# Kernel optimization log

Measured on AMD Instinct MI355X. Metric: run time of the kernel, lower is better.

## Reference

```python
import jax, jax.numpy as jnp
import numpy as np

N_NODES = 4096
N_GRAPHS = 128
D_IN = 128
HEADS = 4
KEY_SIZE = 32  # == num_channels
D_OUT = 32 * D_IN  # num_channels * irreps.dim


def setup_inputs() -> dict:
    key = jax.random.key(0)
    ks = jax.random.split(key, 5)
    nodes = jax.random.normal(ks[0], (N_NODES, D_IN), dtype=jnp.float32)
    # 128 graphs of 32 nodes each, packed: sum(n_node) == N_NODES
    n_node = jnp.full((N_GRAPHS,), N_NODES // N_GRAPHS, dtype=jnp.int32)
    s_in = 1.0 / np.sqrt(D_IN)
    s_h = 1.0 / np.sqrt(HEADS * KEY_SIZE)
    Wq = jax.random.normal(ks[1], (D_IN, HEADS, KEY_SIZE), dtype=jnp.float32) * s_in
    Wk = jax.random.normal(ks[2], (D_IN, HEADS, KEY_SIZE), dtype=jnp.float32) * s_in
    Wv = jax.random.normal(ks[3], (D_IN, HEADS, KEY_SIZE), dtype=jnp.float32) * s_in
    Wo = jax.random.normal(ks[4], (HEADS * KEY_SIZE, D_OUT), dtype=jnp.float32) * s_h
    bq = jnp.zeros((HEADS, KEY_SIZE), dtype=jnp.float32)
    bk = jnp.zeros((HEADS, KEY_SIZE), dtype=jnp.float32)
    bv = jnp.zeros((HEADS, KEY_SIZE), dtype=jnp.float32)
    bo = jnp.zeros((D_OUT,), dtype=jnp.float32)
    return {"nodes": nodes, "n_node": n_node, "Wq": Wq, "bq": bq,
            "Wk": Wk, "bk": bk, "Wv": Wv, "bv": bv, "Wo": Wo, "bo": bo}


def reference(nodes, n_node, Wq, bq, Wk, bk, Wv, bv, Wo, bo):
    N = nodes.shape[0]
    G = n_node.shape[0]
    # segment id per packed node (get_segment_ids)
    seg = jnp.repeat(jnp.arange(G), n_node, total_repeat_length=N)
    # per-head projections: [N, H, K]
    q = jnp.einsum('nd,dhk->nhk', nodes, Wq) + bq
    k = jnp.einsum('nd,dhk->nhk', nodes, Wk) + bk
    v = jnp.einsum('nd,dhk->nhk', nodes, Wv) + bv
    # dense logits masked to block-diagonal per-graph blocks: [H, N, N]
    logits = jnp.einsum('nhk,mhk->hnm', q, k) / jnp.sqrt(jnp.float32(KEY_SIZE))
    mask = seg[:, None] == seg[None, :]  # [N, N]
    logits = jnp.where(mask[None, :, :], logits, jnp.float32(-1e30))
    attn = jax.nn.softmax(logits, axis=-1)
    out = jnp.einsum('hnm,mhk->nhk', attn, v).reshape(N, HEADS * KEY_SIZE)
    return out @ Wo + bo  # [N, num_channels * d_in]
```

## Files before the change

### kernel.cpp

```cpp
#include <hip/hip_runtime.h>
#include <hip/hip_bf16.h>


typedef __attribute__((ext_vector_type(4))) float f32x4;
typedef __attribute__((ext_vector_type(8))) short s16x8;
typedef __attribute__((ext_vector_type(4))) short s16x4;
typedef __attribute__((ext_vector_type(8))) __bf16 bf16x8;

static __device__ __forceinline__ short f2bf(float f) {
  union { float f; unsigned u; } v; v.f = f;
  unsigned r = v.u + 0x7fffu + ((v.u >> 16) & 1u);
  return (short)(r >> 16);
}

static __device__ __forceinline__ f32x4 mfma16(s16x8 a, s16x8 b, f32x4 c) {
  return __builtin_amdgcn_mfma_f32_16x16x32_bf16(
      __builtin_bit_cast(bf16x8, a), __builtin_bit_cast(bf16x8, b), c, 0, 0, 0);
}

__global__ __launch_bounds__(256) void k0_prep(
    const float* __restrict__ Wq, const float* __restrict__ Wk,
    const float* __restrict__ Wv, const float* __restrict__ Wo,
    unsigned short* __restrict__ WqkvT, unsigned short* __restrict__ WoT)
{
  __shared__ alignas(16) short sT[64][136];
  const int b = blockIdx.x;
  const float* in; unsigned short* out; int C; int n0;
  if (b < 64)      { in = Wo; out = WoT;           C = 4096; n0 = b << 6; }
  else if (b < 66) { in = Wq; out = WqkvT;         C = 128;  n0 = (b - 64) << 6; }
  else if (b < 68) { in = Wk; out = WqkvT + 16384; C = 128;  n0 = (b - 66) << 6; }
  else             { in = Wv; out = WqkvT + 32768; C = 128;  n0 = (b - 68) << 6; }
  const int t  = threadIdx.x;
  const int rr = t >> 4;
  const int c4 = (t & 15) << 2;
  #pragma unroll
  for (int i = 0; i < 8; ++i) {
    int r = i * 16 + rr;
    float4 v = *(const float4*)(in + r * C + n0 + c4);
    sT[c4 + 0][r] = f2bf(v.x);
    sT[c4 + 1][r] = f2bf(v.y);
    sT[c4 + 2][r] = f2bf(v.z);
    sT[c4 + 3][r] = f2bf(v.w);
  }
  __syncthreads();
  const int c  = t >> 2;
  const int k0 = (t & 3) << 5;
  #pragma unroll
  for (int j = 0; j < 4; ++j)
    *(s16x8*)&out[(n0 + c) * 128 + k0 + j * 8] = *(const s16x8*)&sT[c][k0 + j * 8];
}

__global__ __launch_bounds__(64) void k1_qkv_attn(
    const float* __restrict__ nodes,
    const unsigned short* __restrict__ WqkvT,
    const float* __restrict__ bq, const float* __restrict__ bk,
    const float* __restrict__ bv,
    unsigned short* __restrict__ attout)
{
  const int g = blockIdx.x;
  const int h = blockIdx.y;
  const int lane = threadIdx.x;
  const int l15 = lane & 15;
  const int qd = lane >> 4;

  __shared__ alignas(16) short sN[32][136];
  __shared__ alignas(16) short sQ[32][40];
  __shared__ alignas(16) short sK[32][40];
  __shared__ alignas(16) short sVT[32][40];
  __shared__ alignas(16) short sP[32][40];

  const float* ng = nodes + g * 32 * 128;
  #pragma unroll
  for (int i = 0; i < 16; ++i) {
    int f4  = i * 64 + lane;
    int row = f4 >> 5;
    int c4  = (f4 & 31) << 2;
    float4 v = *(const float4*)(ng + row * 128 + c4);
    s16x4 p;
    p[0] = f2bf(v.x); p[1] = f2bf(v.y); p[2] = f2bf(v.z); p[3] = f2bf(v.w);
    *(s16x4*)&sN[row][c4] = p;
  }
  __syncthreads();

  s16x8 afrag[2][4];
  #pragma unroll
  for (int mt = 0; mt < 2; ++mt)
    #pragma unroll
    for (int kk = 0; kk < 4; ++kk)
      afrag[mt][kk] = *(const s16x8*)&sN[mt * 16 + l15][kk * 32 + qd * 8];

  const float* Bm[3] = {bq, bk, bv};

  #pragma unroll
  for (int m3 = 0; m3 < 3; ++m3) {
    const unsigned short* WT = WqkvT + m3 * 16384;
    s16x8 bfr[4][2];
    #pragma unroll
    for (int kk = 0; kk < 4; ++kk)
      #pragma unroll
      for (int nt = 0; nt < 2; ++nt)
        bfr[kk][nt] = *(const s16x8*)&WT[(h * 32 + nt * 16 + l15) * 128 + kk * 32 + qd * 8];
    f32x4 acc[2][2];
    f32x4 zero = {0.f, 0.f, 0.f, 0.f};
    acc[0][0] = zero; acc[0][1] = zero; acc[1][0] = zero; acc[1][1] = zero;
    #pragma unroll
    for (int kk = 0; kk < 4; ++kk)
      #pragma unroll
      for (int mt = 0; mt < 2; ++mt)
        #pragma unroll
        for (int nt = 0; nt < 2; ++nt)
          acc[mt][nt] = mfma16(afrag[mt][kk], bfr[kk][nt], acc[mt][nt]);
    float b0 = Bm[m3][h * 32 + l15];
    float b1 = Bm[m3][h * 32 + 16 + l15];
    #pragma unroll
    for (int mt = 0; mt < 2; ++mt)
      #pragma unroll
      for (int nt = 0; nt < 2; ++nt) {
        float bb = nt ? b1 : b0;
        #pragma unroll
        for (int r = 0; r < 4; ++r) {
          int m = mt * 16 + qd * 4 + r;
          int c = nt * 16 + l15;
          float val = acc[mt][nt][r] + bb;
          if (m3 == 0)      sQ[m][c]  = f2bf(val * 0.17677669529663687f);
          else if (m3 == 1) sK[m][c]  = f2bf(val);
          else              sVT[c][m] = f2bf(val);
        }
      }
  }
  __syncthreads();

  s16x8 qf[2], kf[2];
  #pragma unroll
  for (int mt = 0; mt < 2; ++mt) qf[mt] = *(const s16x8*)&sQ[mt * 16 + l15][qd * 8];
  #pragma unroll
  for (int nt = 0; nt < 2; ++nt) kf[nt] = *(const s16x8*)&sK[nt * 16 + l15][qd * 8];
  f32x4 sacc[2][2];
  {
    f32x4 zero = {0.f, 0.f, 0.f, 0.f};
    #pragma unroll
    for (int mt = 0; mt < 2; ++mt)
      #pragma unroll
      for (int nt = 0; nt < 2; ++nt)
        sacc[mt][nt] = mfma16(qf[mt], kf[nt], zero);
  }

  #pragma unroll
  for (int mt = 0; mt < 2; ++mt)
    #pragma unroll
    for (int r = 0; r < 4; ++r) {
      float a0 = sacc[mt][0][r], a1 = sacc[mt][1][r];
      float mx = fmaxf(a0, a1);
      mx = fmaxf(mx, __shfl_xor(mx, 1, 64));
      mx = fmaxf(mx, __shfl_xor(mx, 2, 64));
      mx = fmaxf(mx, __shfl_xor(mx, 4, 64));
      mx = fmaxf(mx, __shfl_xor(mx, 8, 64));
      float e0 = __expf(a0 - mx), e1 = __expf(a1 - mx);
      float s = e0 + e1;
      s += __shfl_xor(s, 1, 64);
      s += __shfl_xor(s, 2, 64);
      s += __shfl_xor(s, 4, 64);
      s += __shfl_xor(s, 8, 64);
      float inv = 1.0f / s;
      int m = mt * 16 + qd * 4 + r;
      sP[m][l15]      = f2bf(e0 * inv);
      sP[m][16 + l15] = f2bf(e1 * inv);
    }
  __syncthreads();

  s16x8 pf[2], vf[2];
  #pragma unroll
  for (int mt = 0; mt < 2; ++mt) pf[mt] = *(const s16x8*)&sP[mt * 16 + l15][qd * 8];
  #pragma unroll
  for (int nt = 0; nt < 2; ++nt) vf[nt] = *(const s16x8*)&sVT[nt * 16 + l15][qd * 8];
  f32x4 oacc[2][2];
  {
    f32x4 zero = {0.f, 0.f, 0.f, 0.f};
    #pragma unroll
    for (int mt = 0; mt < 2; ++mt)
      #pragma unroll
      for (int nt = 0; nt < 2; ++nt)
        oacc[mt][nt] = mfma16(pf[mt], vf[nt], zero);
  }
  unsigned short* ao = attout + (g * 32) * 128 + h * 32;
  #pragma unroll
  for (int mt = 0; mt < 2; ++mt)
    #pragma unroll
    for (int nt = 0; nt < 2; ++nt)
      #pragma unroll
      for (int r = 0; r < 4; ++r) {
        int m = mt * 16 + qd * 4 + r;
        int c = nt * 16 + l15;
        ao[m * 128 + c] = (unsigned short)f2bf(oacc[mt][nt][r]);
      }
}

__global__ __launch_bounds__(256) void k3_gemm(
    const unsigned short* __restrict__ A,
    const unsigned short* __restrict__ BT,
    const float* __restrict__ bo,
    float* __restrict__ C)
{
  __shared__ alignas(16) short sA[128][136];
  __shared__ alignas(16) short sB[128][136];
  const int t  = threadIdx.x;
  const int m0 = blockIdx.y << 7;
  const int n0 = blockIdx.x << 7;

  #pragma unroll
  for (int i = 0; i < 8; ++i) {
    int id  = i * 256 + t;
    int row = id >> 4;
    int ch  = (id & 15) << 3;
    *(s16x8*)&sA[row][ch] = *(const s16x8*)(A  + (m0 + row) * 128 + ch);
    *(s16x8*)&sB[row][ch] = *(const s16x8*)(BT + (n0 + row) * 128 + ch);
  }
  __syncthreads();

  const int w    = t >> 6;
  const int lane = t & 63;
  const int l15  = lane & 15;
  const int qd   = lane >> 4;
  const int wm   = (w >> 1) << 6;
  const int wn   = (w & 1) << 6;

  f32x4 acc[4][4];
  {
    f32x4 zero = {0.f, 0.f, 0.f, 0.f};
    #pragma unroll
    for (int i = 0; i < 4; ++i)
      #pragma unroll
      for (int j = 0; j < 4; ++j) acc[i][j] = zero;
  }

  #pragma unroll
  for (int kk = 0; kk < 4; ++kk) {
    s16x8 af[4], bf[4];
    #pragma unroll
    for (int i = 0; i < 4; ++i)
      af[i] = *(const s16x8*)&sA[wm + i * 16 + l15][kk * 32 + qd * 8];
    #pragma unroll
    for (int j = 0; j < 4; ++j)
      bf[j] = *(const s16x8*)&sB[wn + j * 16 + l15][kk * 32 + qd * 8];
    #pragma unroll
    for (int i = 0; i < 4; ++i)
      #pragma unroll
      for (int j = 0; j < 4; ++j)
        acc[i][j] = mfma16(af[i], bf[j], acc[i][j]);
  }

  float bov[4];
  #pragma unroll
  for (int j = 0; j < 4; ++j) bov[j] = bo[n0 + wn + j * 16 + l15];

  #pragma unroll
  for (int i = 0; i < 4; ++i) {
    int rbase = m0 + wm + i * 16 + qd * 4;
    #pragma unroll
    for (int r = 0; r < 4; ++r) {
      float* crow = C + (rbase + r) * 4096 + n0 + wn + l15;
      #pragma unroll
      for (int j = 0; j < 4; ++j)
        crow[j * 16] = acc[i][j][r] + bov[j];
    }
  }
}

extern "C" void kernel_launch(void* const* d_in, const int* in_sizes, int n_in,
                              void* d_out, int out_size, void* d_ws, size_t ws_size,
                              hipStream_t stream) {
  const float* nodes = (const float*)d_in[0];
  const float* Wq = (const float*)d_in[2];
  const float* bq = (const float*)d_in[3];
  const float* Wk = (const float*)d_in[4];
  const float* bk = (const float*)d_in[5];
  const float* Wv = (const float*)d_in[6];
  const float* bv = (const float*)d_in[7];
  const float* Wo = (const float*)d_in[8];
  const float* bo = (const float*)d_in[9];
  float* out = (float*)d_out;

  unsigned short* attout = (unsigned short*)d_ws;
  unsigned short* WoT    = attout + 4096 * 128;
  unsigned short* WqkvT  = WoT + 4096 * 128;

  k0_prep<<<70, 256, 0, stream>>>(Wq, Wk, Wv, Wo, WqkvT, WoT);
  k1_qkv_attn<<<dim3(128, 4), 64, 0, stream>>>(nodes, WqkvT, bq, bk, bv, attout);
  k3_gemm<<<dim3(32, 32), 256, 0, stream>>>(attout, WoT, bo, out);
}
```

Measured before the change: 108.7 us.

## Drop LDS staging in output GEMM and use vectorized nontemporal stores

The output projection GEMM now loads MFMA fragments directly from global memory instead of staging tiles through shared memory, removing the barrier and the LDS traffic. The MFMA operands are swapped so each lane holds four consecutive output columns. This allows bias loads and output writes to be 16-byte vector stores, marked nontemporal to avoid polluting the cache with the large 64MB output. The risk is that global fragment loads are less coalesced and rely on L1/L2 for reuse across waves.

```diff
diff --git a/kernel.cpp b/kernel.cpp
--- a/kernel.cpp
+++ b/kernel.cpp
@@ -201,22 +201,9 @@
     const float* __restrict__ bo,
     float* __restrict__ C)
 {
-  __shared__ alignas(16) short sA[128][136];
-  __shared__ alignas(16) short sB[128][136];
-  const int t  = threadIdx.x;
-  const int m0 = blockIdx.y << 7;
-  const int n0 = blockIdx.x << 7;
-
-  #pragma unroll
-  for (int i = 0; i < 8; ++i) {
-    int id  = i * 256 + t;
-    int row = id >> 4;
-    int ch  = (id & 15) << 3;
-    *(s16x8*)&sA[row][ch] = *(const s16x8*)(A  + (m0 + row) * 128 + ch);
-    *(s16x8*)&sB[row][ch] = *(const s16x8*)(BT + (n0 + row) * 128 + ch);
-  }
-  __syncthreads();
-
+  const int t    = threadIdx.x;
+  const int m0   = blockIdx.y << 7;
+  const int n0   = blockIdx.x << 7;
   const int w    = t >> 6;
   const int lane = t & 63;
   const int l15  = lane & 15;
@@ -224,13 +211,16 @@
   const int wm   = (w >> 1) << 6;
   const int wn   = (w & 1) << 6;
 
+  const unsigned short* Ab = A  + (m0 + wm + l15) * 128 + qd * 8;
+  const unsigned short* Bb = BT + (n0 + wn + l15) * 128 + qd * 8;
+
   f32x4 acc[4][4];
   {
     f32x4 zero = {0.f, 0.f, 0.f, 0.f};
     #pragma unroll
-    for (int i = 0; i < 4; ++i)
-      #pragma unroll
-      for (int j = 0; j < 4; ++j) acc[i][j] = zero;
+    for (int j = 0; j < 4; ++j)
+      #pragma unroll
+      for (int i = 0; i < 4; ++i) acc[j][i] = zero;
   }
 
   #pragma unroll
@@ -238,30 +228,29 @@
     s16x8 af[4], bf[4];
     #pragma unroll
     for (int i = 0; i < 4; ++i)
-      af[i] = *(const s16x8*)&sA[wm + i * 16 + l15][kk * 32 + qd * 8];
+      af[i] = *(const s16x8*)(Ab + i * 16 * 128 + kk * 32);
     #pragma unroll
     for (int j = 0; j < 4; ++j)
-      bf[j] = *(const s16x8*)&sB[wn + j * 16 + l15][kk * 32 + qd * 8];
-    #pragma unroll
-    for (int i = 0; i < 4; ++i)
-      #pragma unroll
-      for (int j = 0; j < 4; ++j)
-        acc[i][j] = mfma16(af[i], bf[j], acc[i][j]);
-  }
-
-  float bov[4];
-  #pragma unroll
-  for (int j = 0; j < 4; ++j) bov[j] = bo[n0 + wn + j * 16 + l15];
+      bf[j] = *(const s16x8*)(Bb + j * 16 * 128 + kk * 32);
+    #pragma unroll
+    for (int j = 0; j < 4; ++j)
+      #pragma unroll
+      for (int i = 0; i < 4; ++i)
+        acc[j][i] = mfma16(bf[j], af[i], acc[j][i]);
+  }
+
+  f32x4 bv4[4];
+  #pragma unroll
+  for (int j = 0; j < 4; ++j)
+    bv4[j] = *(const f32x4*)&bo[n0 + wn + j * 16 + qd * 4];
 
   #pragma unroll
   for (int i = 0; i < 4; ++i) {
-    int rbase = m0 + wm + i * 16 + qd * 4;
-    #pragma unroll
-    for (int r = 0; r < 4; ++r) {
-      float* crow = C + (rbase + r) * 4096 + n0 + wn + l15;
-      #pragma unroll
-      for (int j = 0; j < 4; ++j)
-        crow[j * 16] = acc[i][j][r] + bov[j];
+    float* crow = C + (m0 + wm + i * 16 + l15) * 4096 + n0 + wn + qd * 4;
+    #pragma unroll
+    for (int j = 0; j < 4; ++j) {
+      f32x4 v = acc[j][i] + bv4[j];
+      __builtin_nontemporal_store(v, (f32x4*)(crow + j * 16));
     }
   }
 }
```

Result: slower. 120.0 us (+10.4%).
